# Performance work log

Measured on AMD Instinct MI355X. Metric: run time of the kernel, lower is better.

## Reference

```python
import jax, jax.numpy as jnp
import numpy as np

VOXEL_SIZE = 0.4
STRIDE = 2
NUM_BATCH = 4
PRE_MAXSIZE = 1024  # nms_premaxsize
NMS_THR = 0.1
NEG_INF = -1e9


def setup_inputs() -> dict:
    key = jax.random.key(0)
    ks = jax.random.split(key, 7)
    N, C = 200000, 256
    feat = jax.random.normal(ks[0], (N, C), dtype=jnp.float32)
    batch_idx = jax.random.randint(ks[1], (N,), 0, NUM_BATCH, dtype=jnp.int32)
    coor = jax.random.randint(ks[2], (N, 2), 0, 400, dtype=jnp.int32)
    W_cls = jax.random.normal(ks[3], (C, 2), dtype=jnp.float32) * 0.02
    b_cls = jnp.zeros((2,), dtype=jnp.float32)
    W_reg = jax.random.normal(ks[4], (C, 9), dtype=jnp.float32) * 0.02
    b_reg = jnp.zeros((9,), dtype=jnp.float32)
    return {"feat": feat, "batch_idx": batch_idx, "coor": coor,
            "W_cls": W_cls, "b_cls": b_cls, "W_reg": W_reg, "b_reg": b_reg}


def _bev_iou(bx):
    # bx: [K,7] (x,y,z,l,w,h,r); axis-aligned BEV IoU on (x,y,l,w)
    x, y, l, w = bx[:, 0], bx[:, 1], bx[:, 3], bx[:, 4]
    x1, x2 = x - l / 2, x + l / 2
    y1, y2 = y - w / 2, y + w / 2
    ix = jnp.maximum(jnp.minimum(x2[:, None], x2[None, :]) - jnp.maximum(x1[:, None], x1[None, :]), 0.0)
    iy = jnp.maximum(jnp.minimum(y2[:, None], y2[None, :]) - jnp.maximum(y1[:, None], y1[None, :]), 0.0)
    inter = ix * iy
    area = l * w
    union = area[:, None] + area[None, :] - inter
    return inter / jnp.maximum(union, 1e-6)


def _nms_keep(iou):
    # greedy NMS over score-descending rows; returns keep mask [K]
    K = iou.shape[0]
    idx = jnp.arange(K)

    def body(i, supp):
        keep_i = jnp.logical_not(supp[i])
        new = keep_i & (iou[i] > NMS_THR) & (idx > i)
        return supp | new

    supp = jax.lax.fori_loop(0, K, body, jnp.zeros((K,), dtype=bool))
    return jnp.logical_not(supp)


def reference(feat, batch_idx, coor, W_cls, b_cls, W_reg, b_reg):
    # ---- shared heads over all sparse voxels ----
    cls_logits = feat @ W_cls + b_cls            # [N, 1+1] (neg evidence, class)
    probs = jax.nn.softmax(cls_logits, axis=-1)
    cls_prob = probs[:, 1:]                      # [N, n_cls]
    conf = jnp.max(cls_prob, axis=-1)            # [N]
    label = jnp.argmax(cls_prob, axis=-1)        # [N]

    reg = feat @ W_reg + b_reg                   # [N, 9] -> ctr(3) dim(3) dir(2) scr(1)
    ctr, dim, drn, scr = reg[:, :3], reg[:, 3:6], reg[:, 6:8], reg[:, 8]
    scr = jax.nn.sigmoid(scr)                    # sigmoid_keys=['scr']

    # indices2metric: voxel indices -> metric centers
    centers = coor.astype(jnp.float32) * (VOXEL_SIZE * STRIDE)  # [N, 2]

    xy = centers + ctr[:, :2]
    z = ctr[:, 2]
    lwh = jnp.exp(jnp.clip(dim, -6.0, 6.0))
    angle = jnp.arctan2(drn[:, 0], drn[:, 1])
    boxes = jnp.concatenate([xy, z[:, None], lwh, angle[:, None]], axis=-1)  # [N, 7]
    score = conf * scr                           # [N]

    def per_sample(b):
        s = jnp.where(batch_idx == b, score, NEG_INF)
        vals, idx = jax.lax.top_k(s, PRE_MAXSIZE)          # score-sorted (desc)
        bx = boxes[idx]                                     # [K, 7]
        lb = label[idx]                                     # [K]
        valid = vals > NEG_INF / 2
        iou = _bev_iou(bx)
        keep = _nms_keep(iou) & valid
        out = jnp.concatenate([bx, vals[:, None]], axis=-1) * keep[:, None]  # [K, 8]
        return out, lb, keep

    out, lb, keep = jax.vmap(per_sample)(jnp.arange(NUM_BATCH))
    return out, lb, keep
```

## Files before the change

kernel.cpp:

```cpp
#include <hip/hip_runtime.h>
#include <math.h>

#define NBATCH 4
#define PRE 1024
#define CAND 4096
#define NHIST 65536
#define MAXSLOT 384

typedef __attribute__((address_space(1))) const void GlbVoid;
typedef __attribute__((address_space(3))) void LdsVoid;

__device__ __forceinline__ void gld_lds16(const void* g, void* l) {
    __builtin_amdgcn_global_load_lds((GlbVoid*)g, (LdsVoid*)l, 16, 0, 0);
}

__device__ __forceinline__ unsigned long long allow_mask(int i, int l) {
    int base = l << 6;
    if (i < base) return ~0ull;
    int sh = i - base + 1;
    if (sh >= 64) return 0ull;
    return (~0ull) << sh;
}

__global__ void k0_weights(const float* __restrict__ Wcls, const float* __restrict__ bcls,
                           const float* __restrict__ Wreg, const float* __restrict__ breg,
                           double* __restrict__ Wd3, float* __restrict__ Wf8,
                           double* __restrict__ biasD, float* __restrict__ biasF) {
    int j = blockIdx.x;
    int c = threadIdx.x;
    if (j < 2) {
        Wd3[j * 256 + c] = (double)Wcls[c * 2 + j];
        if (c == 0) biasD[j] = (double)bcls[j];
    } else if (j == 10) {
        Wd3[2 * 256 + c] = (double)Wreg[c * 9 + 8];
        if (c == 0) biasD[2] = (double)breg[8];
    } else {
        int r = j - 2;
        Wf8[r * 256 + c] = Wreg[c * 9 + r];
        if (c == 0) biasF[r] = breg[r];
    }
}

__global__ __launch_bounds__(256) void k1_points(
    const float* __restrict__ feat, const int* __restrict__ batch_idx,
    const int* __restrict__ coor, const double* __restrict__ Wd3,
    const float* __restrict__ Wf8, const double* __restrict__ biasD,
    const float* __restrict__ biasF, float* __restrict__ pointData,
    unsigned long long* __restrict__ keys, unsigned int* __restrict__ hist, int N) {
    __shared__ float sbuf[2][256 * 32];
    const int tid = threadIdx.x;
    const int w = tid >> 6, lane = tid & 63;
    const int p0 = blockIdx.x * 256;

    double accD0 = 0.0, accD1 = 0.0, accD2 = 0.0;
    float accF[8];
#pragma unroll
    for (int j = 0; j < 8; ++j) accF[j] = 0.f;

    const int s_src = (lane & 7) ^ (lane >> 3);

    auto stage = [&](int buf, int ch) {
#pragma unroll
        for (int it = 0; it < 8; ++it) {
            int R0 = w * 64 + it * 8;
            int r = R0 + (lane >> 3);
            int gp = p0 + r;
            if (gp >= N) gp = N - 1;
            const float* g = feat + (size_t)gp * 256 + ch * 32 + s_src * 4;
            gld_lds16(g, &sbuf[buf][R0 * 32]);
        }
    };

    auto compute = [&](int buf, int ch) {
        const float* row = &sbuf[buf][tid * 32];
        const int rs = tid & 7;
#pragma unroll
        for (int k4 = 0; k4 < 8; ++k4) {
            const float4 v = *(const float4*)(row + ((k4 ^ rs) * 4));
            const int cb = ch * 32 + k4 * 4;
            float vv[4] = {v.x, v.y, v.z, v.w};
#pragma unroll
            for (int m = 0; m < 4; ++m) {
                int c = cb + m;
                double fd = (double)vv[m];
                accD0 = fma(fd, Wd3[c], accD0);
                accD1 = fma(fd, Wd3[256 + c], accD1);
                accD2 = fma(fd, Wd3[512 + c], accD2);
#pragma unroll
                for (int j = 0; j < 8; ++j) accF[j] = fmaf(vv[m], Wf8[j * 256 + c], accF[j]);
            }
        }
    };

    stage(0, 0);
    __syncthreads();
    for (int ch = 0; ch < 8; ++ch) {
        if (ch < 7) stage((ch + 1) & 1, ch + 1);
        compute(ch & 1, ch);
        __syncthreads();
    }

    int gp = p0 + tid;
    if (gp < N) {
        double d0 = biasD[0] + accD0, d1 = biasD[1] + accD1, d2 = biasD[2] + accD2;
        float f[8];
#pragma unroll
        for (int j = 0; j < 8; ++j) f[j] = biasF[j] + accF[j];
        double conf = 1.0 / (1.0 + exp(-(d1 - d0)));
        double scr = 1.0 / (1.0 + exp(-d2));
        double score = conf * scr;
        float s32 = (float)score;

        float cx = (float)coor[2 * gp] * 0.8f;
        float cy = (float)coor[2 * gp + 1] * 0.8f;
        float bx = cx + f[0], by = cy + f[1], bz = f[2];
        float bl = expf(fminf(fmaxf(f[3], -6.f), 6.f));
        float bw = expf(fminf(fmaxf(f[4], -6.f), 6.f));
        float bh = expf(fminf(fmaxf(f[5], -6.f), 6.f));
        float ba = atan2f(f[6], f[7]);

        float4* pd = (float4*)(pointData + (size_t)gp * 8);
        pd[0] = make_float4(bx, by, bz, bl);
        pd[1] = make_float4(bw, bh, ba, s32);
        keys[gp] = (unsigned long long)__double_as_longlong(score);
        int b = batch_idx[gp];
        atomicAdd(&hist[b * NHIST + (__float_as_uint(s32) >> 16)], 1u);
    }
}

__global__ __launch_bounds__(256) void k2_thresh(const unsigned int* __restrict__ hist,
                                                 unsigned int* __restrict__ Tarr) {
    int b = blockIdx.x, tid = threadIdx.x;
    __shared__ unsigned int csum[256];
    __shared__ unsigned int chunkv[256];
    __shared__ int stc;
    __shared__ unsigned int scum;
    const unsigned int* h = hist + b * NHIST;
    unsigned int s = 0;
    for (int m = 0; m < 256; ++m) s += h[tid * 256 + m];
    csum[tid] = s;
    __syncthreads();
    if (tid == 0) {
        unsigned int cum = 0; int tc = -1;
        for (int t = 255; t >= 0; --t) {
            if (cum + csum[t] >= 1024u) { tc = t; break; }
            cum += csum[t];
        }
        stc = tc; scum = cum;
    }
    __syncthreads();
    int tc = stc;
    if (tc < 0) { if (tid == 0) Tarr[b] = 0u; return; }
    chunkv[tid] = h[tc * 256 + tid];
    __syncthreads();
    if (tid == 0) {
        unsigned int cum = scum, T = (unsigned int)(tc * 256);
        for (int m = 255; m >= 0; --m) {
            unsigned int c = chunkv[m];
            if (cum + c >= 1024u) { T = (unsigned int)(tc * 256 + m); break; }
            cum += c;
        }
        Tarr[b] = T;
    }
}

__global__ void k3_compact(const int* __restrict__ batch_idx, const float* __restrict__ pointData,
                           const unsigned long long* __restrict__ keys,
                           const unsigned int* __restrict__ Tarr, unsigned int* __restrict__ candCount,
                           unsigned int* __restrict__ candIdx, unsigned long long* __restrict__ candKey,
                           int N) {
    int p = blockIdx.x * 256 + threadIdx.x;
    if (p >= N) return;
    int b = batch_idx[p];
    float s32 = pointData[(size_t)p * 8 + 7];
    unsigned int bucket = __float_as_uint(s32) >> 16;
    if (bucket >= Tarr[b]) {
        unsigned int pos = atomicAdd(&candCount[b], 1u);
        if (pos < CAND) {
            candIdx[b * CAND + pos] = (unsigned int)p;
            candKey[b * CAND + pos] = keys[p];
        }
    }
}

__global__ __launch_bounds__(1024) void k4_sort(const unsigned int* __restrict__ candCount,
                                                const unsigned int* __restrict__ candIdx,
                                                const unsigned long long* __restrict__ candKey,
                                                const float* __restrict__ pointData,
                                                float* __restrict__ topBox,
                                                unsigned int* __restrict__ validArr) {
    int b = blockIdx.x, tid = threadIdx.x;
    __shared__ unsigned long long ka[CAND];
    __shared__ unsigned int id[CAND];
    unsigned int cnt = candCount[b];
    if (cnt > CAND) cnt = CAND;
    int n = (cnt <= 2048u) ? 2048 : 4096;
    for (int t = tid; t < n; t += 1024) {
        if ((unsigned int)t < cnt) {
            ka[t] = ~candKey[b * CAND + t];
            id[t] = candIdx[b * CAND + t];
        } else {
            ka[t] = ~0ull;
            id[t] = 0xFFFFFFFFu;
        }
    }
    __syncthreads();
    for (int k = 2; k <= n; k <<= 1) {
        for (int j = k >> 1; j > 0; j >>= 1) {
            for (int t = tid; t < n; t += 1024) {
                int l = t ^ j;
                if (l > t) {
                    bool up = ((t & k) == 0);
                    unsigned long long kt = ka[t], kl = ka[l];
                    unsigned int it_ = id[t], il = id[l];
                    bool gt = (kt > kl) || (kt == kl && it_ > il);
                    if (gt == up) { ka[t] = kl; ka[l] = kt; id[t] = il; id[l] = it_; }
                }
            }
            __syncthreads();
        }
    }
    unsigned int gi = id[tid];
    bool valid = (gi != 0xFFFFFFFFu) && ((unsigned int)tid < cnt);
    float v[8];
#pragma unroll
    for (int k = 0; k < 8; ++k) v[k] = 0.f;
    if (valid) {
        const float* pd = pointData + (size_t)gi * 8;
#pragma unroll
        for (int k = 0; k < 8; ++k) v[k] = pd[k];
    }
    float* tb = topBox + (size_t)(b * PRE + tid) * 8;
#pragma unroll
    for (int k = 0; k < 8; ++k) tb[k] = v[k];
    validArr[b * PRE + tid] = valid ? 1u : 0u;
}

__global__ __launch_bounds__(256) void k5_iou(const float* __restrict__ topBox,
                                              unsigned long long* __restrict__ M) {
    int wid = blockIdx.x * 4 + (threadIdx.x >> 6);
    int lane = threadIdx.x & 63;
    int b = wid >> 14;
    int rem = wid & 16383;
    int i = rem >> 4;
    int wj = rem & 15;
    if (wj < (i >> 6)) return;
    const float* bi = topBox + (size_t)(b * PRE + i) * 8;
    int j = wj * 64 + lane;
    const float* bj = topBox + (size_t)(b * PRE + j) * 8;
    float xi = bi[0], yi = bi[1], li = bi[3], wi_ = bi[4];
    float xj = bj[0], yj = bj[1], lj = bj[3], wj_ = bj[4];
    float x1i = xi - li * 0.5f, x2i = xi + li * 0.5f;
    float y1i = yi - wi_ * 0.5f, y2i = yi + wi_ * 0.5f;
    float x1j = xj - lj * 0.5f, x2j = xj + lj * 0.5f;
    float y1j = yj - wj_ * 0.5f, y2j = yj + wj_ * 0.5f;
    float ix = fmaxf(fminf(x2i, x2j) - fmaxf(x1i, x1j), 0.0f);
    float iy = fmaxf(fminf(y2i, y2j) - fmaxf(y1i, y1j), 0.0f);
    float inter = ix * iy;
    float ai = li * wi_, aj = lj * wj_;
    float uni = ai + aj - inter;
    float iou = inter / fmaxf(uni, 1e-6f);
    unsigned long long m = __ballot(iou > 0.1f);
    if (lane == 0) M[(size_t)(b * PRE + i) * 16 + wj] = m;
}

__global__ __launch_bounds__(256) void k6_nms(const unsigned long long* __restrict__ M,
                                              const unsigned int* __restrict__ validArr,
                                              const float* __restrict__ topBox,
                                              float* __restrict__ out0,
                                              float* __restrict__ keepOut) {
    __shared__ unsigned long long Mc[MAXSLOT * 16];
    __shared__ unsigned int slotIdx[PRE];
    __shared__ unsigned int cntSh;
    __shared__ unsigned long long suppSh[16];
    int b = blockIdx.x, tid = threadIdx.x;
    if (tid == 0) cntSh = 0;
    __syncthreads();
    for (int r = tid; r < PRE; r += 256) {
        const unsigned long long* row = M + (size_t)(b * PRE + r) * 16;
        unsigned long long w[16];
        unsigned long long o = 0ull;
#pragma unroll
        for (int l = 0; l < 16; ++l) { w[l] = row[l] & allow_mask(r, l); o |= w[l]; }
        unsigned int s = 0xFFFFFFFFu;
        if (o != 0ull) {
            unsigned int slot = atomicAdd(&cntSh, 1u);
            if (slot < MAXSLOT) {
                s = slot;
#pragma unroll
                for (int l = 0; l < 16; ++l) Mc[slot * 16 + l] = w[l];
            } else s = 0xFFFFFFFEu;
        }
        slotIdx[r] = s;
    }
    __syncthreads();
    if (tid < 64) {
        int lane = tid;
        unsigned long long supp = 0ull;
        for (int g = 0; g < 16; ++g) {
            unsigned long long act = __ballot(slotIdx[g * 64 + lane] != 0xFFFFFFFFu);
            while (act) {
                int bit = __builtin_ctzll(act);
                act &= act - 1ull;
                int i = g * 64 + bit;
                unsigned long long wsup = __shfl(supp, g);
                bool keep_i = ((wsup >> (i & 63)) & 1ull) == 0ull;
                if (keep_i && lane < 16) {
                    unsigned int s = slotIdx[i];
                    unsigned long long add = (s < MAXSLOT)
                        ? Mc[s * 16 + lane]
                        : (M[(size_t)(b * PRE + i) * 16 + lane] & allow_mask(i, lane));
                    supp |= add;
                }
            }
        }
        if (lane < 16) suppSh[lane] = supp;
    }
    __syncthreads();
    for (int r = tid; r < PRE; r += 256) {
        bool keep = (((suppSh[r >> 6] >> (r & 63)) & 1ull) == 0ull) && (validArr[b * PRE + r] != 0u);
        float kf = keep ? 1.0f : 0.0f;
        const float* tb = topBox + (size_t)(b * PRE + r) * 8;
        float* o = out0 + (size_t)(b * PRE + r) * 8;
#pragma unroll
        for (int k = 0; k < 8; ++k) o[k] = tb[k] * kf;
        keepOut[b * PRE + r] = kf;
    }
}

extern "C" void kernel_launch(void* const* d_in, const int* in_sizes, int n_in,
                              void* d_out, int out_size, void* d_ws, size_t ws_size,
                              hipStream_t stream) {
    int N = in_sizes[0] / 256;
    const float* feat = (const float*)d_in[0];
    const int* batch_idx = (const int*)d_in[1];
    const int* coor = (const int*)d_in[2];
    const float* Wcls = (const float*)d_in[3];
    const float* bcls = (const float*)d_in[4];
    const float* Wreg = (const float*)d_in[5];
    const float* breg = (const float*)d_in[6];

    char* ws = (char*)d_ws;
    size_t off = 0;
    auto take = [&](size_t bytes) -> char* {
        char* r = ws + off;
        off += (bytes + 255) & ~(size_t)255;
        return r;
    };
    float* pointData = (float*)take((size_t)N * 8 * 4);
    unsigned long long* keys = (unsigned long long*)take((size_t)N * 8);
    unsigned int* hist = (unsigned int*)take((size_t)NBATCH * NHIST * 4);
    unsigned int* Tarr = (unsigned int*)take(NBATCH * 4);
    unsigned int* candCount = (unsigned int*)take(NBATCH * 4);
    unsigned int* candIdx = (unsigned int*)take(NBATCH * CAND * 4);
    unsigned long long* candKey = (unsigned long long*)take(NBATCH * CAND * 8);
    float* topBox = (float*)take(NBATCH * PRE * 8 * 4);
    unsigned int* validArr = (unsigned int*)take(NBATCH * PRE * 4);
    unsigned long long* M = (unsigned long long*)take((size_t)NBATCH * PRE * 16 * 8);
    double* Wd3 = (double*)take(3 * 256 * 8);
    float* Wf8 = (float*)take(8 * 256 * 4);
    double* biasD = (double*)take(3 * 8);
    float* biasF = (float*)take(8 * 4);

    float* out0 = (float*)d_out;
    float* keepOut = out0 + NBATCH * PRE * 8 + NBATCH * PRE;

    hipMemsetAsync(d_out, 0, (size_t)out_size * 4, stream);
    hipMemsetAsync(hist, 0, (size_t)NBATCH * NHIST * 4, stream);
    hipMemsetAsync(candCount, 0, NBATCH * 4, stream);

    int pbPts = (N + 255) / 256;
    k0_weights<<<dim3(11), dim3(256), 0, stream>>>(Wcls, bcls, Wreg, breg, Wd3, Wf8, biasD, biasF);
    k1_points<<<dim3(pbPts), dim3(256), 0, stream>>>(feat, batch_idx, coor,
                                                     Wd3, Wf8, biasD, biasF,
                                                     pointData, keys, hist, N);
    k2_thresh<<<dim3(NBATCH), dim3(256), 0, stream>>>(hist, Tarr);
    k3_compact<<<dim3(pbPts), dim3(256), 0, stream>>>(batch_idx, pointData, keys, Tarr,
                                                      candCount, candIdx, candKey, N);
    k4_sort<<<dim3(NBATCH), dim3(1024), 0, stream>>>(candCount, candIdx, candKey,
                                                     pointData, topBox, validArr);
    k5_iou<<<dim3(NBATCH * PRE * 16 / 4), dim3(256), 0, stream>>>(topBox, M);
    k6_nms<<<dim3(NBATCH), dim3(256), 0, stream>>>(M, validArr, topBox, out0, keepOut);
}
```

Measured before the change: 470.0 us.

## Aggregate compaction atomics per wavefront, merge memsets, split point kernel launch

The compaction kernel now uses a ballot per batch so one lane issues a single atomicAdd for the whole wavefront, and each lane computes its slot with a popcount prefix. This is meant to cut contention on the four global counters. The candidate counter is moved next to the histogram so one memset clears both, dropping one API call. The point kernel is also launched as two half-grids with a block offset, which adds a launch and may change how the work is scheduled.

New measurement: 511.3 us. +8.8%, slower.

```diff
diff --git a/kernel.cpp b/kernel.cpp
--- a/kernel.cpp
+++ b/kernel.cpp
@@ -46,11 +46,12 @@
     const int* __restrict__ coor, const double* __restrict__ Wd3,
     const float* __restrict__ Wf8, const double* __restrict__ biasD,
     const float* __restrict__ biasF, float* __restrict__ pointData,
-    unsigned long long* __restrict__ keys, unsigned int* __restrict__ hist, int N) {
+    unsigned long long* __restrict__ keys, unsigned int* __restrict__ hist,
+    int N, int boff) {
     __shared__ float sbuf[2][256 * 32];
     const int tid = threadIdx.x;
     const int w = tid >> 6, lane = tid & 63;
-    const int p0 = blockIdx.x * 256;
+    const int p0 = (blockIdx.x + boff) * 256;
 
     double accD0 = 0.0, accD1 = 0.0, accD2 = 0.0;
     float accF[8];
@@ -170,15 +171,30 @@
                            unsigned int* __restrict__ candIdx, unsigned long long* __restrict__ candKey,
                            int N) {
     int p = blockIdx.x * 256 + threadIdx.x;
-    if (p >= N) return;
-    int b = batch_idx[p];
-    float s32 = pointData[(size_t)p * 8 + 7];
-    unsigned int bucket = __float_as_uint(s32) >> 16;
-    if (bucket >= Tarr[b]) {
-        unsigned int pos = atomicAdd(&candCount[b], 1u);
-        if (pos < CAND) {
-            candIdx[b * CAND + pos] = (unsigned int)p;
-            candKey[b * CAND + pos] = keys[p];
+    int lane = threadIdx.x & 63;
+    bool pred = false;
+    int b = 0;
+    if (p < N) {
+        b = batch_idx[p];
+        float s32 = pointData[(size_t)p * 8 + 7];
+        unsigned int bucket = __float_as_uint(s32) >> 16;
+        pred = (bucket >= Tarr[b]);
+    }
+#pragma unroll
+    for (int bb = 0; bb < NBATCH; ++bb) {
+        unsigned long long mk = __ballot(pred && (b == bb));
+        if (mk != 0ull) {
+            int leader = __ffsll((long long)mk) - 1;
+            unsigned int base = 0;
+            if (lane == leader) base = atomicAdd(&candCount[bb], (unsigned int)__popcll(mk));
+            base = (unsigned int)__shfl((int)base, leader);
+            if (pred && (b == bb)) {
+                unsigned int pos = base + (unsigned int)__popcll(mk & ((1ull << lane) - 1ull));
+                if (pos < CAND) {
+                    candIdx[bb * CAND + pos] = (unsigned int)p;
+                    candKey[bb * CAND + pos] = keys[p];
+                }
+            }
         }
     }
 }
@@ -350,8 +366,8 @@
     float* pointData = (float*)take((size_t)N * 8 * 4);
     unsigned long long* keys = (unsigned long long*)take((size_t)N * 8);
     unsigned int* hist = (unsigned int*)take((size_t)NBATCH * NHIST * 4);
+    unsigned int* candCount = (unsigned int*)take(NBATCH * 4);
     unsigned int* Tarr = (unsigned int*)take(NBATCH * 4);
-    unsigned int* candCount = (unsigned int*)take(NBATCH * 4);
     unsigned int* candIdx = (unsigned int*)take(NBATCH * CAND * 4);
     unsigned long long* candKey = (unsigned long long*)take(NBATCH * CAND * 8);
     float* topBox = (float*)take(NBATCH * PRE * 8 * 4);
@@ -366,17 +382,21 @@
     float* keepOut = out0 + NBATCH * PRE * 8 + NBATCH * PRE;
 
     hipMemsetAsync(d_out, 0, (size_t)out_size * 4, stream);
-    hipMemsetAsync(hist, 0, (size_t)NBATCH * NHIST * 4, stream);
-    hipMemsetAsync(candCount, 0, NBATCH * 4, stream);
-
-    int pbPts = (N + 255) / 256;
+    hipMemsetAsync(hist, 0, (size_t)NBATCH * NHIST * 4 + NBATCH * 4, stream);
+
+    int nb = (N + 255) / 256;
+    int nb1 = nb / 2;
+    int nb2 = nb - nb1;
     k0_weights<<<dim3(11), dim3(256), 0, stream>>>(Wcls, bcls, Wreg, breg, Wd3, Wf8, biasD, biasF);
-    k1_points<<<dim3(pbPts), dim3(256), 0, stream>>>(feat, batch_idx, coor,
-                                                     Wd3, Wf8, biasD, biasF,
-                                                     pointData, keys, hist, N);
+    k1_points<<<dim3(nb1), dim3(256), 0, stream>>>(feat, batch_idx, coor,
+                                                   Wd3, Wf8, biasD, biasF,
+                                                   pointData, keys, hist, N, 0);
+    k1_points<<<dim3(nb2), dim3(256), 0, stream>>>(feat, batch_idx, coor,
+                                                   Wd3, Wf8, biasD, biasF,
+                                                   pointData, keys, hist, N, nb1);
     k2_thresh<<<dim3(NBATCH), dim3(256), 0, stream>>>(hist, Tarr);
-    k3_compact<<<dim3(pbPts), dim3(256), 0, stream>>>(batch_idx, pointData, keys, Tarr,
-                                                      candCount, candIdx, candKey, N);
+    k3_compact<<<dim3(nb), dim3(256), 0, stream>>>(batch_idx, pointData, keys, Tarr,
+                                                   candCount, candIdx, candKey, N);
     k4_sort<<<dim3(NBATCH), dim3(1024), 0, stream>>>(candCount, candIdx, candKey,
                                                      pointData, topBox, validArr);
     k5_iou<<<dim3(NBATCH * PRE * 16 / 4), dim3(256), 0, stream>>>(topBox, M);
```
